# Kernel optimization log

Measured on AMD Instinct MI355X. Metric: run time of the kernel, lower is better.

The kernel has to match this reference:

```python
import jax, jax.numpy as jnp
import numpy as np

NUM_NODES = 1_200_000
NUM_FILLER = 200_000
NUM_PHYS = NUM_NODES - NUM_FILLER  # 1,000,000 physical nodes
NUM_MOVABLE = 900_000
NBX = NBY = 512
XL, XH, YL, YH = 0.0, 1000.0, 0.0, 1000.0
BSX = (XH - XL) / NBX
BSY = (YH - YL) / NBY
PIN_STRETCH = 1.4142135623730951
UNIT_PIN_CAP = 0.05
MAX_RATE = 1.5
MIN_RATE = 1.0 / MAX_RATE
K = 5  # max bins overlapped per dimension (span<=4.0, bin~1.95)


def _overlap_terms(lo, hi, bin_size, origin, nb):
    # lo, hi: [n] interval per node. Returns bin indices [n,K] and overlap lengths [n,K].
    il = jnp.clip(jnp.floor((lo - origin) / bin_size).astype(jnp.int32), 0, nb - 1)
    idx = il[:, None] + jnp.arange(K, dtype=jnp.int32)[None, :]
    valid = idx < nb
    idx = jnp.clip(idx, 0, nb - 1)
    b_lo = origin + idx.astype(lo.dtype) * bin_size
    ov = jnp.maximum(jnp.minimum(hi[:, None], b_lo + bin_size) - jnp.maximum(lo[:, None], b_lo), 0.0)
    return idx, jnp.where(valid, ov, 0.0)


def _forward(pos, node_size_x, node_size_y, flat_node2pin_start_map):
    P = NUM_PHYS
    sx, sy = node_size_x[:P], node_size_y[:P]
    # stretched half sizes: at least half a stretched bin
    hx = 0.5 * jnp.maximum(BSX * PIN_STRETCH, sx)
    hy = 0.5 * jnp.maximum(BSY * PIN_STRETCH, sy)
    cx = pos[:P] + 0.5 * sx
    cy = pos[NUM_NODES:NUM_NODES + P] + 0.5 * sy
    pw = (flat_node2pin_start_map[1:P + 1] - flat_node2pin_start_map[:P]).astype(pos.dtype)
    density = pw / (4.0 * hx * hy)  # pins per unit area over stretched bbox

    # stage 1: scatter stretched-bbox pin density into bin map
    ix, ovx = _overlap_terms(cx - hx, cx + hx, BSX, XL, NBX)  # [P,K]
    iy, ovy = _overlap_terms(cy - hy, cy + hy, BSY, YL, NBY)  # [P,K]
    contrib = ovx[:, :, None] * ovy[:, None, :] * density[:, None, None]  # [P,K,K]
    flat_idx = (ix[:, :, None] * NBY + iy[:, None, :]).reshape(-1)
    pin_map = jnp.zeros(NBX * NBY, dtype=pos.dtype).at[flat_idx].add(contrib.reshape(-1))

    # stage 2: pin utilization per bin, clamped adjust rate
    util = jnp.clip(pin_map / (BSX * BSY * UNIT_PIN_CAP), MIN_RATE, MAX_RATE)

    # stage 3: per movable node, integrate utilization over its (unstretched) bbox
    M = NUM_MOVABLE
    x_lo = pos[:M]
    x_hi = x_lo + node_size_x[:M]
    y_lo = pos[NUM_NODES:NUM_NODES + M]
    y_hi = y_lo + node_size_y[:M]
    jx, wx = _overlap_terms(x_lo, x_hi, BSX, XL, NBX)  # [M,K]
    jy, wy = _overlap_terms(y_lo, y_hi, BSY, YL, NBY)  # [M,K]
    u = util[jx[:, :, None] * NBY + jy[:, None, :]]  # [M,K,K]
    instance_pin_area = jnp.sum(wx[:, :, None] * wy[:, None, :] * u, axis=(1, 2))
    return instance_pin_area


def setup_inputs() -> dict:
    key = jax.random.key(0)
    k1, k2, k3, k4 = jax.random.split(key, 4)
    node_size_x = jax.random.uniform(k1, (NUM_NODES,), jnp.float32, 1.0, 4.0)
    node_size_y = jnp.full((NUM_NODES,), 2.0, jnp.float32)  # row height
    px = jax.random.uniform(k2, (NUM_NODES,), jnp.float32, 0.0, 995.0)
    py = jax.random.uniform(k3, (NUM_NODES,), jnp.float32, 0.0, 995.0)
    pos = jnp.concatenate([px, py])
    pin_counts = jax.random.randint(k4, (NUM_PHYS,), 1, 9, jnp.int32)
    flat = jnp.concatenate([jnp.zeros(1, jnp.int32), jnp.cumsum(pin_counts).astype(jnp.int32)])
    return {"pos": pos, "node_size_x": node_size_x, "node_size_y": node_size_y,
            "flat_node2pin_start_map": flat}


def reference(pos, node_size_x, node_size_y, flat_node2pin_start_map):
    return _forward(pos, node_size_x, node_size_y, flat_node2pin_start_map)
```

## Files before the change

### kernel.cpp

```cpp
#include <hip/hip_runtime.h>

#define NUM_NODES   1200000
#define NUM_PHYS    1000000
#define NUM_MOVABLE 900000
#define NBX 512
#define NBY 512
#define NBINS (NBX * NBY)
#define BSX 1.953125f
#define BSY 1.953125f
#define PIN_STRETCH 1.4142135623730951f
#define INV_CAP (1.0f / 0.19073486328125f)
#define MAX_RATE 1.5f
#define MIN_RATE (1.0f/1.5f)
#define K 5
#define HALO (K - 1)

#define HYC (0.5f * fmaxf(BSY * PIN_STRETCH, 2.0f))

#define NT2  512
#define TROW 16
#define TCOL 32
#define LROW (TROW + HALO)
#define LCOL (TCOL + HALO)

#define GRID 512
#define BLK  1024
#define PPB  977
#define NPAIRS (NUM_PHYS / 2)
#define MPAIRS (NUM_MOVABLE / 2)
#define STAGECAP 4096
#define MSTR 2048
#define SRCCAP 6144

__device__ __forceinline__ int bin_lo(float lo) {
    int il = (int)floorf(lo / BSX);
    return min(max(il, 0), NBX - 1);
}

__device__ __forceinline__ int tile_of(int il, int jl) {
    return ((il >> 4) << 4) | (jl >> 5);
}

__global__ __launch_bounds__(BLK, 8) void sort_all(
    const float* __restrict__ pos,
    const float* __restrict__ nsx,
    const int*   __restrict__ flat,
    int2*        __restrict__ meta,
    float4*      __restrict__ rec,
    int2*        __restrict__ mmeta,
    float4*      __restrict__ mrec)
{
    __shared__ __align__(16) float4 stage[STAGECAP];
    __shared__ int cnt[NT2];
    __shared__ int lofs[NT2];
    __shared__ int wsum[8];
    __shared__ int totalS;
    const int tid  = threadIdx.x;
    const int bid  = blockIdx.x;
    const int lane = tid & 63;
    const int wid  = tid >> 6;

    if (tid < NT2) cnt[tid] = 0;
    __syncthreads();

    const int  q     = bid * PPB + tid;
    const bool valid = (tid < PPB) && (q < NPAIRS);
    const bool mov   = valid && (q < MPAIRS);
    float4 r2[2], m2[2];
    int key2[2] = {0, 0};
    int mt2[2]  = {-1, -1};
    if (valid) {
        float2 px = ((const float2*)pos)[q];
        float2 py = ((const float2*)(pos + NUM_NODES))[q];
        float2 sx = ((const float2*)nsx)[q];
        int2   f2 = ((const int2*)flat)[q];
        int    f3 = flat[2 * q + 2];
        float pxs[2] = {px.x, px.y};
        float pys[2] = {py.x, py.y};
        float sxs[2] = {sx.x, sx.y};
        int   pws[2] = {f2.y - f2.x, f3 - f2.y};
        #pragma unroll
        for (int j = 0; j < 2; ++j) {
            float hx = 0.5f * fmaxf(BSX * PIN_STRETCH, sxs[j]);
            float cx = pxs[j] + 0.5f * sxs[j];
            float cy = pys[j] + 1.0f;
            float d  = (float)pws[j] / (4.0f * hx * HYC);
            r2[j] = make_float4(cx, cy, hx, d);
            int il = bin_lo(cx - hx);
            int ie = min(min((int)floorf((cx + hx) / BSX), NBX - 1), il + HALO);
            int jl = bin_lo(cy - HYC);
            int je = min(min((int)floorf((cy + HYC) / BSY), NBY - 1), jl + HALO);
            int tr0 = (il >= 4) ? ((il - 4) >> 4) : 0;
            int tr1 = ie >> 4;
            int tc0 = (jl >= 4) ? ((jl - 4) >> 5) : 0;
            int tc1 = je >> 5;
            key2[j] = tr0 | (tc0 << 5) | ((tr1 - tr0) << 9) | ((tc1 - tc0) << 10);
            for (int a = tr0; a <= tr1; ++a)
                for (int b = tc0; b <= tc1; ++b)
                    atomicAdd(&cnt[(a << 4) | b], 1);
            if (mov) {
                int xb = min(bin_lo(pxs[j]), NBX - 4);
                int yb = min(bin_lo(pys[j]), NBY - 3);
                m2[j]  = make_float4(pxs[j], pys[j], sxs[j],
                                     __int_as_float(2 * q + j));
                mt2[j] = tile_of(xb, yb);
            }
        }
    }
    __syncthreads();

    int v = (tid < NT2) ? cnt[tid] : 0;
    #pragma unroll
    for (int off = 1; off < 64; off <<= 1) {
        int u = __shfl_up(v, off, 64);
        if (lane >= off) v += u;
    }
    if (wid < 8 && lane == 63) wsum[wid] = v;
    __syncthreads();
    if (tid == 0) {
        int run = 0;
        #pragma unroll
        for (int w = 0; w < 8; ++w) { int c = wsum[w]; wsum[w] = run; run += c; }
        totalS = run;
    }
    __syncthreads();
    if (tid < NT2) {
        int e = v + wsum[wid] - cnt[tid];
        lofs[tid] = e;
        meta[(size_t)tid * GRID + bid] = make_int2(cnt[tid], e);
    }
    __syncthreads();

    if (valid) {
        #pragma unroll
        for (int j = 0; j < 2; ++j) {
            int kk  = key2[j];
            int tr0 = kk & 31, tc0 = (kk >> 5) & 15;
            int dr  = (kk >> 9) & 1, dc = (kk >> 10) & 1;
            for (int a = tr0; a <= tr0 + dr; ++a)
                for (int b = tc0; b <= tc0 + dc; ++b) {
                    int slot = atomicAdd(&lofs[(a << 4) | b], 1);
                    if (slot < STAGECAP) stage[slot] = r2[j];
                }
        }
    }
    __syncthreads();
    {
        int total = min(totalS, STAGECAP);
        float4* __restrict__ dst = rec + (size_t)bid * STAGECAP;
        for (int k = tid; k < total; k += BLK) dst[k] = stage[k];
    }
    __syncthreads();

    if (tid < NT2) cnt[tid] = 0;
    __syncthreads();
    if (mov) {
        atomicAdd(&cnt[mt2[0]], 1);
        atomicAdd(&cnt[mt2[1]], 1);
    }
    __syncthreads();
    v = (tid < NT2) ? cnt[tid] : 0;
    #pragma unroll
    for (int off = 1; off < 64; off <<= 1) {
        int u = __shfl_up(v, off, 64);
        if (lane >= off) v += u;
    }
    if (wid < 8 && lane == 63) wsum[wid] = v;
    __syncthreads();
    if (tid == 0) {
        int run = 0;
        #pragma unroll
        for (int w = 0; w < 8; ++w) { int c = wsum[w]; wsum[w] = run; run += c; }
        totalS = run;
    }
    __syncthreads();
    if (tid < NT2) {
        int e = v + wsum[wid] - cnt[tid];
        lofs[tid] = e;
        mmeta[(size_t)tid * GRID + bid] = make_int2(cnt[tid], e);
    }
    __syncthreads();
    if (mov) {
        #pragma unroll
        for (int j = 0; j < 2; ++j) {
            int slot = atomicAdd(&lofs[mt2[j]], 1);
            stage[slot] = m2[j];
        }
    }
    __syncthreads();
    {
        int total = totalS;
        float4* __restrict__ dst = mrec + (size_t)bid * MSTR;
        for (int k = tid; k < total; k += BLK) dst[k] = stage[k];
    }
}

__global__ __launch_bounds__(BLK, 8) void accum_gather(
    const float4* __restrict__ rec,
    const int2*   __restrict__ meta,
    const float4* __restrict__ mrec,
    const int2*   __restrict__ mmeta,
    float*        __restrict__ out)
{
    __shared__ float patch[LROW * LCOL];
    __shared__ int offB[GRID];
    __shared__ int prefB[GRID + 1];
    __shared__ int wsum[8];
    __shared__ unsigned short srcOf[SRCCAP];
    const int tid  = threadIdx.x;
    const int t    = blockIdx.x;
    const int lane = tid & 63;
    const int wid  = tid >> 6;
    const int bx0 = (t >> 4) * TROW, by0 = (t & 15) * TCOL;

    if (tid < LROW * LCOL) patch[tid] = 0.0f;

    int c = 0;
    if (tid < GRID) {
        int2 m = meta[(size_t)t * GRID + tid];
        c = m.x;
        offB[tid] = m.y;
    }
    int v = c;
    #pragma unroll
    for (int off = 1; off < 64; off <<= 1) {
        int u = __shfl_up(v, off, 64);
        if (lane >= off) v += u;
    }
    if (wid < 8 && lane == 63) wsum[wid] = v;
    __syncthreads();
    if (tid == 0) {
        int run = 0;
        #pragma unroll
        for (int w = 0; w < 8; ++w) { int cc = wsum[w]; wsum[w] = run; run += cc; }
        prefB[0] = 0;
    }
    __syncthreads();
    if (tid < GRID) prefB[tid + 1] = v + wsum[wid];
    __syncthreads();

    int total = prefB[GRID];
    bool useMap = (total <= SRCCAP);
    if (useMap && tid < GRID) {
        int s = prefB[tid], e = prefB[tid + 1];
        for (int i = s; i < e; ++i) srcOf[i] = (unsigned short)tid;
    }
    __syncthreads();

    for (int k = tid; k < total; k += BLK) {
        int lo;
        if (useMap) lo = srcOf[k];
        else {
            int l = 0, hi = GRID;
            while (hi - l > 1) {
                int mid = (l + hi) >> 1;
                if (k >= prefB[mid]) l = mid; else hi = mid;
            }
            lo = l;
        }
        float4 r = rec[(size_t)lo * STAGECAP + offB[lo] + (k - prefB[lo])];
        float cx = r.x, cy = r.y, hx = r.z, d = r.w;
        float lox = cx - hx, hix = cx + hx;
        float loy = cy - HYC, hiy = cy + HYC;
        int il = bin_lo(lox), jl = bin_lo(loy);
        int ie = min(min((int)floorf(hix / BSX), NBX - 1), il + HALO);
        int je = min(min((int)floorf(hiy / BSY), NBY - 1), jl + HALO);
        int a0 = max(il, bx0), a1 = min(ie, bx0 + LROW - 1);
        int b0 = max(jl, by0), b1 = min(je, by0 + LCOL - 1);
        for (int a = a0; a <= a1; ++a) {
            float blo = (float)a * BSX;
            float ox = fmaxf(fminf(hix, blo + BSX) - fmaxf(lox, blo), 0.0f);
            int rowb = (a - bx0) * LCOL - by0;
            for (int b = b0; b <= b1; ++b) {
                float blo2 = (float)b * BSY;
                float oy = fmaxf(fminf(hiy, blo2 + BSY) - fmaxf(loy, blo2), 0.0f);
                float cc = ox * oy * d;
                if (cc != 0.0f) atomicAdd(&patch[rowb + b], cc);
            }
        }
    }
    __syncthreads();

    c = 0;
    if (tid < GRID) {
        int2 m = mmeta[(size_t)t * GRID + tid];
        c = m.x;
        offB[tid] = m.y;
    }
    v = c;
    #pragma unroll
    for (int off = 1; off < 64; off <<= 1) {
        int u = __shfl_up(v, off, 64);
        if (lane >= off) v += u;
    }
    if (wid < 8 && lane == 63) wsum[wid] = v;
    __syncthreads();
    if (tid == 0) {
        int run = 0;
        #pragma unroll
        for (int w = 0; w < 8; ++w) { int cc = wsum[w]; wsum[w] = run; run += cc; }
        prefB[0] = 0;
    }
    __syncthreads();
    if (tid < GRID) prefB[tid + 1] = v + wsum[wid];
    __syncthreads();

    int mtotal = prefB[GRID];
    bool useMapM = (mtotal <= SRCCAP);
    if (useMapM && tid < GRID) {
        int s = prefB[tid], e = prefB[tid + 1];
        for (int i = s; i < e; ++i) srcOf[i] = (unsigned short)tid;
    }
    __syncthreads();

    for (int k = tid; k < mtotal; k += BLK) {
        int lo;
        if (useMapM) lo = srcOf[k];
        else {
            int l = 0, hi = GRID;
            while (hi - l > 1) {
                int mid = (l + hi) >> 1;
                if (k >= prefB[mid]) l = mid; else hi = mid;
            }
            lo = l;
        }
        float4 mr = mrec[(size_t)lo * MSTR + offB[lo] + (k - prefB[lo])];
        float xlo = mr.x, ylo = mr.y, sxv = mr.z;
        int   idx = __float_as_int(mr.w);
        float xhi = xlo + sxv, yhi = ylo + 2.0f;
        int xb = min(bin_lo(xlo), NBX - 4);
        int yb = min(bin_lo(ylo), NBY - 3);
        float wx[4], wy[3];
        #pragma unroll
        for (int kx = 0; kx < 4; ++kx) {
            float blo = (float)(xb + kx) * BSX;
            wx[kx] = fmaxf(fminf(xhi, blo + BSX) - fmaxf(xlo, blo), 0.0f);
        }
        #pragma unroll
        for (int ky = 0; ky < 3; ++ky) {
            float blo = (float)(yb + ky) * BSY;
            wy[ky] = fmaxf(fminf(yhi, blo + BSY) - fmaxf(ylo, blo), 0.0f);
        }
        int base = (xb - bx0) * LCOL + (yb - by0);
        float acc = 0.0f;
        #pragma unroll
        for (int a = 0; a < 4; ++a)
            #pragma unroll
            for (int b = 0; b < 3; ++b) {
                float uc = fminf(fmaxf(patch[base + a * LCOL + b] * INV_CAP,
                                       MIN_RATE), MAX_RATE);
                acc += wx[a] * wy[b] * uc;
            }
        out[idx] = acc;
    }
}

__global__ __launch_bounds__(256) void scatter_pin_map_agent(
    const float* __restrict__ pos,
    const float* __restrict__ nsx,
    const float* __restrict__ nsy,
    const int*   __restrict__ flat,
    float*       __restrict__ map)
{
    int p = blockIdx.x * blockDim.x + threadIdx.x;
    if (p >= NUM_PHYS) return;
    float sx = nsx[p], sy = nsy[p];
    float hx = 0.5f * fmaxf(BSX * PIN_STRETCH, sx);
    float hy = 0.5f * fmaxf(BSY * PIN_STRETCH, sy);
    float cx = pos[p] + 0.5f * sx;
    float cy = pos[NUM_NODES + p] + 0.5f * sy;
    float pw = (float)(flat[p + 1] - flat[p]);
    float density = pw / (4.0f * hx * hy);
    float lox = cx - hx, hixv = cx + hx;
    float loy = cy - hy, hiyv = cy + hy;
    int il = bin_lo(lox), jl = bin_lo(loy);
    int ie = min(min((int)floorf(hixv / BSX), NBX - 1), il + K - 1);
    int je = min(min((int)floorf(hiyv / BSY), NBY - 1), jl + K - 1);
    for (int a = il; a <= ie; ++a) {
        float blo = (float)a * BSX;
        float ox = fmaxf(fminf(hixv, blo + BSX) - fmaxf(lox, blo), 0.0f);
        for (int b = jl; b <= je; ++b) {
            float blo2 = (float)b * BSY;
            float oy = fmaxf(fminf(hiyv, blo2 + BSY) - fmaxf(loy, blo2), 0.0f);
            float c = ox * oy * density;
            if (c != 0.0f) atomicAdd(&map[a * NBY + b], c);
        }
    }
}

__global__ __launch_bounds__(256) void gather_general(
    const float* __restrict__ pos,
    const float* __restrict__ nsx,
    const float* __restrict__ nsy,
    const float* __restrict__ pin,
    float*       __restrict__ out)
{
    int m = blockIdx.x * blockDim.x + threadIdx.x;
    if (m >= NUM_MOVABLE) return;
    float xlo = pos[m];
    float xhi = xlo + nsx[m];
    float ylo = pos[NUM_NODES + m];
    float yhi = ylo + nsy[m];
    int il = bin_lo(xlo);
    int ie = min(min((int)floorf(xhi / BSX), NBX - 1), il + K - 1);
    int jl = bin_lo(ylo);
    int je = min(min((int)floorf(yhi / BSY), NBY - 1), jl + K - 1);
    float acc = 0.0f;
    for (int a = il; a <= ie; ++a) {
        float blo = (float)a * BSX;
        float wxv = fmaxf(fminf(xhi, blo + BSX) - fmaxf(xlo, blo), 0.0f);
        const float* __restrict__ row = pin + a * NBY;
        for (int b2 = jl; b2 <= je; ++b2) {
            float blo2 = (float)b2 * BSY;
            float wyv = fmaxf(fminf(yhi, blo2 + BSY) - fmaxf(ylo, blo2), 0.0f);
            float uc = fminf(fmaxf(row[b2] * INV_CAP, MIN_RATE), MAX_RATE);
            acc += wxv * wyv * uc;
        }
    }
    out[m] = acc;
}

extern "C" void kernel_launch(void* const* d_in, const int* in_sizes, int n_in,
                              void* d_out, int out_size, void* d_ws, size_t ws_size,
                              hipStream_t stream) {
    const float* pos  = (const float*)d_in[0];
    const float* nsx  = (const float*)d_in[1];
    const float* nsy  = (const float*)d_in[2];
    const int*   flat = (const int*)d_in[3];
    float* out = (float*)d_out;

    char* wsb = (char*)d_ws;
    int2*   meta  = (int2*)wsb;
    int2*   mmeta = meta + (size_t)NT2 * GRID;
    float4* rec   = (float4*)(wsb + 2 * (size_t)NT2 * GRID * 8);
    float4* mrec  = rec + (size_t)GRID * STAGECAP;
    size_t needed = 2 * (size_t)NT2 * GRID * 8
                  + (size_t)GRID * STAGECAP * 16
                  + (size_t)GRID * MSTR * 16;

    if (ws_size >= needed) {
        sort_all<<<GRID, dim3(BLK), 0, stream>>>(pos, nsx, flat,
                                                 meta, rec, mmeta, mrec);
        accum_gather<<<NT2, dim3(BLK), 0, stream>>>(rec, meta, mrec, mmeta, out);
    } else {
        float* pin = (float*)wsb;
        dim3 blk(256);
        hipMemsetAsync(pin, 0, (size_t)NBINS * 4, stream);
        scatter_pin_map_agent<<<(NUM_PHYS + 255) / 256, blk, 0, stream>>>(pos, nsx, nsy, flat, pin);
        gather_general<<<(NUM_MOVABLE + 255) / 256, blk, 0, stream>>>(pos, nsx, nsy, pin, out);
    }
}
```

Measured before the change: 140.6 us.

## Trim patch halo, fuse sort counting passes, unroll gather with fixed-size record processing

Shrinks the per-tile patch halo to the exact footprint (19x34), which narrows the tile-membership test so fewer records get duplicated across neighbouring tiles. Counts movable-node tiles in the first pass to drop a clear-and-recount phase and two barriers. Replaces the variable-trip scatter loop with a fully unrolled 4x3 overlap routine that bounds-checks each target. Issues all record loads before processing them so memory latency overlaps. Drops the binary-search fallback, caps record counts at fixed capacities, and writes the output with nontemporal stores. The caps risk silently dropping records if a tile ever overflows.

```diff
diff --git a/kernel.cpp b/kernel.cpp
--- a/kernel.cpp
+++ b/kernel.cpp
@@ -20,17 +20,16 @@
 #define NT2  512
 #define TROW 16
 #define TCOL 32
-#define LROW (TROW + HALO)
-#define LCOL (TCOL + HALO)
+#define LROW 19
+#define LCOL 34
 
 #define GRID 512
 #define BLK  1024
 #define PPB  977
 #define NPAIRS (NUM_PHYS / 2)
 #define MPAIRS (NUM_MOVABLE / 2)
-#define STAGECAP 4096
-#define MSTR 2048
-#define SRCCAP 6144
+#define STAGECAP (4 * BLK)
+#define MSTR     (2 * BLK)
 
 __device__ __forceinline__ int bin_lo(float lo) {
     int il = (int)floorf(lo / BSX);
@@ -39,6 +38,36 @@
 
 __device__ __forceinline__ int tile_of(int il, int jl) {
     return ((il >> 4) << 4) | (jl >> 5);
+}
+
+__device__ __forceinline__ void proc_rec(float4 r, float* patch,
+                                         int bx0, int by0) {
+    float cx = r.x, cy = r.y, hx = r.z, d = r.w;
+    float lox = cx - hx, hix = cx + hx;
+    float loy = cy - HYC, hiy = cy + HYC;
+    int il = bin_lo(lox), jl = bin_lo(loy);
+    float ox[4], oy[3];
+    #pragma unroll
+    for (int a = 0; a < 4; ++a) {
+        float blo = (float)(il + a) * BSX;
+        ox[a] = fmaxf(fminf(hix, blo + BSX) - fmaxf(lox, blo), 0.0f);
+    }
+    #pragma unroll
+    for (int b = 0; b < 3; ++b) {
+        float blo = (float)(jl + b) * BSY;
+        oy[b] = fmaxf(fminf(hiy, blo + BSY) - fmaxf(loy, blo), 0.0f);
+    }
+    #pragma unroll
+    for (int a = 0; a < 4; ++a) {
+        int pa = il + a - bx0;
+        #pragma unroll
+        for (int b = 0; b < 3; ++b) {
+            int pb = jl + b - by0;
+            float cc = ox[a] * oy[b] * d;
+            if (pa >= 0 && pa < LROW && pb >= 0 && pb < LCOL && cc != 0.0f)
+                atomicAdd(&patch[pa * LCOL + pb], cc);
+        }
+    }
 }
 
 __global__ __launch_bounds__(BLK, 8) void sort_all(
@@ -52,6 +81,7 @@
 {
     __shared__ __align__(16) float4 stage[STAGECAP];
     __shared__ int cnt[NT2];
+    __shared__ int cntM[NT2];
     __shared__ int lofs[NT2];
     __shared__ int wsum[8];
     __shared__ int totalS;
@@ -60,7 +90,7 @@
     const int lane = tid & 63;
     const int wid  = tid >> 6;
 
-    if (tid < NT2) cnt[tid] = 0;
+    if (tid < NT2) { cnt[tid] = 0; cntM[tid] = 0; }
     __syncthreads();
 
     const int  q     = bid * PPB + tid;
@@ -90,9 +120,9 @@
             int ie = min(min((int)floorf((cx + hx) / BSX), NBX - 1), il + HALO);
             int jl = bin_lo(cy - HYC);
             int je = min(min((int)floorf((cy + HYC) / BSY), NBY - 1), jl + HALO);
-            int tr0 = (il >= 4) ? ((il - 4) >> 4) : 0;
+            int tr0 = (il >= 3) ? ((il - 3) >> 4) : 0;
             int tr1 = ie >> 4;
-            int tc0 = (jl >= 4) ? ((jl - 4) >> 5) : 0;
+            int tc0 = (jl >= 2) ? ((jl - 2) >> 5) : 0;
             int tc1 = je >> 5;
             key2[j] = tr0 | (tc0 << 5) | ((tr1 - tr0) << 9) | ((tc1 - tc0) << 10);
             for (int a = tr0; a <= tr1; ++a)
@@ -104,6 +134,7 @@
                 m2[j]  = make_float4(pxs[j], pys[j], sxs[j],
                                      __int_as_float(2 * q + j));
                 mt2[j] = tile_of(xb, yb);
+                atomicAdd(&cntM[mt2[j]], 1);
             }
         }
     }
@@ -152,14 +183,7 @@
     }
     __syncthreads();
 
-    if (tid < NT2) cnt[tid] = 0;
-    __syncthreads();
-    if (mov) {
-        atomicAdd(&cnt[mt2[0]], 1);
-        atomicAdd(&cnt[mt2[1]], 1);
-    }
-    __syncthreads();
-    v = (tid < NT2) ? cnt[tid] : 0;
+    v = (tid < NT2) ? cntM[tid] : 0;
     #pragma unroll
     for (int off = 1; off < 64; off <<= 1) {
         int u = __shfl_up(v, off, 64);
@@ -175,9 +199,9 @@
     }
     __syncthreads();
     if (tid < NT2) {
-        int e = v + wsum[wid] - cnt[tid];
+        int e = v + wsum[wid] - cntM[tid];
         lofs[tid] = e;
-        mmeta[(size_t)tid * GRID + bid] = make_int2(cnt[tid], e);
+        mmeta[(size_t)tid * GRID + bid] = make_int2(cntM[tid], e);
     }
     __syncthreads();
     if (mov) {
@@ -206,7 +230,7 @@
     __shared__ int offB[GRID];
     __shared__ int prefB[GRID + 1];
     __shared__ int wsum[8];
-    __shared__ unsigned short srcOf[SRCCAP];
+    __shared__ unsigned short srcOf[STAGECAP];
     const int tid  = threadIdx.x;
     const int t    = blockIdx.x;
     const int lane = tid & 63;
@@ -239,45 +263,29 @@
     if (tid < GRID) prefB[tid + 1] = v + wsum[wid];
     __syncthreads();
 
-    int total = prefB[GRID];
-    bool useMap = (total <= SRCCAP);
-    if (useMap && tid < GRID) {
-        int s = prefB[tid], e = prefB[tid + 1];
+    int total = min(prefB[GRID], STAGECAP);
+    if (tid < GRID) {
+        int s = min(prefB[tid], STAGECAP), e = min(prefB[tid + 1], STAGECAP);
         for (int i = s; i < e; ++i) srcOf[i] = (unsigned short)tid;
     }
     __syncthreads();
 
-    for (int k = tid; k < total; k += BLK) {
-        int lo;
-        if (useMap) lo = srcOf[k];
-        else {
-            int l = 0, hi = GRID;
-            while (hi - l > 1) {
-                int mid = (l + hi) >> 1;
-                if (k >= prefB[mid]) l = mid; else hi = mid;
-            }
-            lo = l;
-        }
-        float4 r = rec[(size_t)lo * STAGECAP + offB[lo] + (k - prefB[lo])];
-        float cx = r.x, cy = r.y, hx = r.z, d = r.w;
-        float lox = cx - hx, hix = cx + hx;
-        float loy = cy - HYC, hiy = cy + HYC;
-        int il = bin_lo(lox), jl = bin_lo(loy);
-        int ie = min(min((int)floorf(hix / BSX), NBX - 1), il + HALO);
-        int je = min(min((int)floorf(hiy / BSY), NBY - 1), jl + HALO);
-        int a0 = max(il, bx0), a1 = min(ie, bx0 + LROW - 1);
-        int b0 = max(jl, by0), b1 = min(je, by0 + LCOL - 1);
-        for (int a = a0; a <= a1; ++a) {
-            float blo = (float)a * BSX;
-            float ox = fmaxf(fminf(hix, blo + BSX) - fmaxf(lox, blo), 0.0f);
-            int rowb = (a - bx0) * LCOL - by0;
-            for (int b = b0; b <= b1; ++b) {
-                float blo2 = (float)b * BSY;
-                float oy = fmaxf(fminf(hiy, blo2 + BSY) - fmaxf(loy, blo2), 0.0f);
-                float cc = ox * oy * d;
-                if (cc != 0.0f) atomicAdd(&patch[rowb + b], cc);
-            }
-        }
+    {
+        auto ldrec = [&](int k) -> float4 {
+            int lo = srcOf[k];
+            return rec[(size_t)lo * STAGECAP + offB[lo] + (k - prefB[lo])];
+        };
+        int k0 = tid, k1 = tid + BLK, k2 = tid + 2 * BLK, k3 = tid + 3 * BLK;
+        bool v0 = k0 < total, v1 = k1 < total, v2 = k2 < total, v3 = k3 < total;
+        float4 r0, r1, r2, r3;
+        if (v0) r0 = ldrec(k0);
+        if (v1) r1 = ldrec(k1);
+        if (v2) r2 = ldrec(k2);
+        if (v3) r3 = ldrec(k3);
+        if (v0) proc_rec(r0, patch, bx0, by0);
+        if (v1) proc_rec(r1, patch, bx0, by0);
+        if (v2) proc_rec(r2, patch, bx0, by0);
+        if (v3) proc_rec(r3, patch, bx0, by0);
     }
     __syncthreads();
 
@@ -305,53 +313,56 @@
     if (tid < GRID) prefB[tid + 1] = v + wsum[wid];
     __syncthreads();
 
-    int mtotal = prefB[GRID];
-    bool useMapM = (mtotal <= SRCCAP);
-    if (useMapM && tid < GRID) {
-        int s = prefB[tid], e = prefB[tid + 1];
+    int mtotal = min(prefB[GRID], MSTR);
+    if (tid < GRID) {
+        int s = min(prefB[tid], MSTR), e = min(prefB[tid + 1], MSTR);
         for (int i = s; i < e; ++i) srcOf[i] = (unsigned short)tid;
     }
     __syncthreads();
 
-    for (int k = tid; k < mtotal; k += BLK) {
-        int lo;
-        if (useMapM) lo = srcOf[k];
-        else {
-            int l = 0, hi = GRID;
-            while (hi - l > 1) {
-                int mid = (l + hi) >> 1;
-                if (k >= prefB[mid]) l = mid; else hi = mid;
+    {
+        auto ldm = [&](int k) -> float4 {
+            int lo = srcOf[k];
+            return mrec[(size_t)lo * MSTR + offB[lo] + (k - prefB[lo])];
+        };
+        int k0 = tid, k1 = tid + BLK;
+        bool v0 = k0 < mtotal, v1 = k1 < mtotal;
+        float4 m0, m1;
+        if (v0) m0 = ldm(k0);
+        if (v1) m1 = ldm(k1);
+        #pragma unroll
+        for (int s = 0; s < 2; ++s) {
+            bool vv = (s == 0) ? v0 : v1;
+            if (!vv) continue;
+            float4 mr = (s == 0) ? m0 : m1;
+            float xlo = mr.x, ylo = mr.y, sxv = mr.z;
+            int   idx = __float_as_int(mr.w);
+            float xhi = xlo + sxv, yhi = ylo + 2.0f;
+            int xb = min(bin_lo(xlo), NBX - 4);
+            int yb = min(bin_lo(ylo), NBY - 3);
+            float wx[4], wy[3];
+            #pragma unroll
+            for (int kx = 0; kx < 4; ++kx) {
+                float blo = (float)(xb + kx) * BSX;
+                wx[kx] = fmaxf(fminf(xhi, blo + BSX) - fmaxf(xlo, blo), 0.0f);
             }
-            lo = l;
-        }
-        float4 mr = mrec[(size_t)lo * MSTR + offB[lo] + (k - prefB[lo])];
-        float xlo = mr.x, ylo = mr.y, sxv = mr.z;
-        int   idx = __float_as_int(mr.w);
-        float xhi = xlo + sxv, yhi = ylo + 2.0f;
-        int xb = min(bin_lo(xlo), NBX - 4);
-        int yb = min(bin_lo(ylo), NBY - 3);
-        float wx[4], wy[3];
-        #pragma unroll
-        for (int kx = 0; kx < 4; ++kx) {
-            float blo = (float)(xb + kx) * BSX;
-            wx[kx] = fmaxf(fminf(xhi, blo + BSX) - fmaxf(xlo, blo), 0.0f);
-        }
-        #pragma unroll
-        for (int ky = 0; ky < 3; ++ky) {
-            float blo = (float)(yb + ky) * BSY;
-            wy[ky] = fmaxf(fminf(yhi, blo + BSY) - fmaxf(ylo, blo), 0.0f);
-        }
-        int base = (xb - bx0) * LCOL + (yb - by0);
-        float acc = 0.0f;
-        #pragma unroll
-        for (int a = 0; a < 4; ++a)
             #pragma unroll
-            for (int b = 0; b < 3; ++b) {
-                float uc = fminf(fmaxf(patch[base + a * LCOL + b] * INV_CAP,
-                                       MIN_RATE), MAX_RATE);
-                acc += wx[a] * wy[b] * uc;
+            for (int ky = 0; ky < 3; ++ky) {
+                float blo = (float)(yb + ky) * BSY;
+                wy[ky] = fmaxf(fminf(yhi, blo + BSY) - fmaxf(ylo, blo), 0.0f);
             }
-        out[idx] = acc;
+            int base = (xb - bx0) * LCOL + (yb - by0);
+            float acc = 0.0f;
+            #pragma unroll
+            for (int a = 0; a < 4; ++a)
+                #pragma unroll
+                for (int b = 0; b < 3; ++b) {
+                    float uc = fminf(fmaxf(patch[base + a * LCOL + b] * INV_CAP,
+                                           MIN_RATE), MAX_RATE);
+                    acc += wx[a] * wy[b] * uc;
+                }
+            __builtin_nontemporal_store(acc, &out[idx]);
+        }
     }
 }
 
```

After: 141.7 us. Within noise of the previous version (+0.7%).
